# Optimization experiments

Measured on AMD Instinct MI355X. Metric: run time of the kernel, lower is better.

The kernel has to match this reference:

```python
import jax, jax.numpy as jnp
import numpy as np

B, T, E = 4, 2048, 1024
H = 16
DH = E // H
SCALE = DH ** -0.5


def setup_inputs() -> dict:
    key = jax.random.key(0)
    ks = jax.random.split(key, 5)
    # small init scale for weights to keep softmax well-conditioned
    return {
        "x": jax.random.normal(ks[0], (B, T, E), dtype=jnp.float32),
        "w_qkv": jax.random.normal(ks[1], (3 * E, E), dtype=jnp.float32) * 0.02,
        "b_qkv": jax.random.normal(ks[2], (3 * E,), dtype=jnp.float32) * 0.02,
        "w_proj": jax.random.normal(ks[3], (E, E), dtype=jnp.float32) * 0.02,
        "b_proj": jax.random.normal(ks[4], (E,), dtype=jnp.float32) * 0.02,
    }


def reference(x, w_qkv, b_qkv, w_proj, b_proj):
    Bs, Ts, Es = x.shape
    # fused qkv projection (torch Linear: y = x W^T + b)
    qkv = x @ w_qkv.T + b_qkv                       # [B,T,3E]
    qkv = qkv.reshape(Bs, Ts, 3, H, DH)
    q, k, v = qkv[:, :, 0], qkv[:, :, 1], qkv[:, :, 2]  # [B,T,H,DH]
    # scores: materialize full TxT matrix per head, as in the original
    scores = jnp.einsum("bthd,bshd->bhts", q, k) * SCALE  # [B,H,T,T]
    causal = jnp.tril(jnp.ones((Ts, Ts), dtype=bool))
    scores = jnp.where(causal[None, None], scores, jnp.float32(-jnp.inf))
    attn = jax.nn.softmax(scores, axis=-1)
    # dropout = 0.0 (eval / deterministic reference)
    out = jnp.einsum("bhts,bshd->bthd", attn, v)    # [B,T,H,DH]
    out = out.reshape(Bs, Ts, Es)
    return out @ w_proj.T + b_proj
```

## Files before the change

### kernel.cpp

```cpp
#include <hip/hip_runtime.h>
#include <hip/hip_bf16.h>

#define B_ 4
#define T_ 2048
#define E_ 1024
#define H_ 16
#define DH_ 64
#define QSCALE_ 0.18033688f

typedef __attribute__((ext_vector_type(8))) short bf16x8;
typedef __attribute__((ext_vector_type(4))) float f32x4;
typedef unsigned int u32;

__device__ inline ushort f2bf(float f) {
    union { float f; unsigned u; } v; v.f = f;
    unsigned r = (v.u + 0x7fffu + ((v.u >> 16) & 1u)) >> 16;
    return (ushort)r;
}

__device__ inline u32 pack2bf(float a, float b) {
    union { float f; u32 u; } ua, ub; ua.f = a; ub.f = b;
    return __builtin_amdgcn_perm(ub.u, ua.u, 0x07060302);
}

__device__ inline void gload16(const ushort* g, ushort* l) {
    __builtin_amdgcn_global_load_lds((const __attribute__((address_space(1))) u32*)g,
                                     (__attribute__((address_space(3))) u32*)l, 16, 0, 0);
}

__global__ void cvt_all(const float* __restrict__ x, const float* __restrict__ wq,
                        const float* __restrict__ wp,
                        ushort* __restrict__ xo, ushort* __restrict__ wqo, ushort* __restrict__ wpo)
{
    const int NX = B_ * T_ * E_ / 4;
    const int NW = 3 * E_ * E_ / 4;
    int i = blockIdx.x * 256 + threadIdx.x;
    const float* s; ushort* d; int off;
    if (i < NX)            { s = x;  d = xo;  off = i; }
    else if (i < NX + NW)  { s = wq; d = wqo; off = i - NX; }
    else                   { s = wp; d = wpo; off = i - NX - NW; }
    float4 f = ((const float4*)s)[off];
    ushort4 u;
    u.x = f2bf(f.x); u.y = f2bf(f.y); u.z = f2bf(f.z); u.w = f2bf(f.w);
    ((ushort4*)d)[off] = u;
}

__global__ __launch_bounds__(256) void gemm_qkv(
    const ushort* __restrict__ Xb, const ushort* __restrict__ Wb,
    const float* __restrict__ bias,
    ushort* __restrict__ Q, ushort* __restrict__ K, ushort* __restrict__ Vt)
{
    __shared__ ushort As[128 * 64];
    __shared__ ushort Bs[128 * 64];
    const int m0 = blockIdx.x * 128;
    const int n0 = blockIdx.y * 128;
    const int kind = n0 >> 10;
    const int tid  = threadIdx.x;
    const int wave = tid >> 6, lane = tid & 63;
    const int lrow = lane & 15, quad = lane >> 4;
    const int srow8 = lane >> 3;
    const int scol8 = ((lane & 7) ^ srow8) * 8;

    const ushort* gA = Xb + (size_t)(m0 + wave * 8 + srow8) * 1024 + scol8;
    const ushort* gB = Wb + (size_t)(n0 + wave * 8 + srow8) * 1024 + scol8;

    const int mw = (wave >> 1) * 64, nw = (wave & 1) * 64;
    const int rsw = (lrow & 7);

    f32x4 acc[4][4];
#pragma unroll
    for (int i = 0; i < 4; i++)
#pragma unroll
        for (int j = 0; j < 4; j++) acc[i][j] = f32x4{0.f, 0.f, 0.f, 0.f};

    const int b = m0 >> 11;
    const bool ct = (kind != 2);

    for (int k0 = 0; k0 < 1024; k0 += 64) {
        __syncthreads();
#pragma unroll
        for (int g = 0; g < 4; g++) {
            gload16(gA + (size_t)g * 32 * 1024 + k0, &As[(g * 32 + wave * 8) * 64]);
            gload16(gB + (size_t)g * 32 * 1024 + k0, &Bs[(g * 32 + wave * 8) * 64]);
        }
        __syncthreads();
#pragma unroll
        for (int ks = 0; ks < 2; ks++) {
            const int usw = ((ks * 4 + quad) ^ rsw) * 8;
            bf16x8 a[4], bfr[4];
#pragma unroll
            for (int i = 0; i < 4; i++)
                a[i] = *(const bf16x8*)&As[(mw + i * 16 + lrow) * 64 + usw];
#pragma unroll
            for (int j = 0; j < 4; j++)
                bfr[j] = *(const bf16x8*)&Bs[(nw + j * 16 + lrow) * 64 + usw];
            if (ct) {
#pragma unroll
                for (int i = 0; i < 4; i++)
#pragma unroll
                    for (int j = 0; j < 4; j++)
                        acc[i][j] = __builtin_amdgcn_mfma_f32_16x16x32_bf16(bfr[j], a[i], acc[i][j], 0, 0, 0);
            } else {
#pragma unroll
                for (int i = 0; i < 4; i++)
#pragma unroll
                    for (int j = 0; j < 4; j++)
                        acc[i][j] = __builtin_amdgcn_mfma_f32_16x16x32_bf16(a[i], bfr[j], acc[i][j], 0, 0, 0);
            }
        }
    }

    if (ct) {
        ushort* dst = (kind == 0) ? Q : K;
        const float scale = (kind == 0) ? QSCALE_ : 1.f;
#pragma unroll
        for (int j = 0; j < 4; j++) {
            int nq = (n0 & 1023) + nw + j * 16 + quad * 4;
            int h = nq >> 6, d = nq & 63;
            float4 bv = *(const float4*)&bias[n0 + nw + j * 16 + quad * 4];
            size_t bh = (size_t)(b * H_ + h);
#pragma unroll
            for (int i = 0; i < 4; i++) {
                int t = (m0 + mw + i * 16 + lrow) & 2047;
                ushort4 o;
                o.x = f2bf((acc[i][j][0] + bv.x) * scale);
                o.y = f2bf((acc[i][j][1] + bv.y) * scale);
                o.z = f2bf((acc[i][j][2] + bv.z) * scale);
                o.w = f2bf((acc[i][j][3] + bv.w) * scale);
                *(ushort4*)&dst[(bh * T_ + t) * DH_ + d] = o;
            }
        }
    } else {
#pragma unroll
        for (int j = 0; j < 4; j++) {
            int nv = (n0 & 1023) + nw + j * 16 + lrow;
            int h = nv >> 6, d = nv & 63;
            float bv = bias[n0 + nw + j * 16 + lrow];
            size_t bh = (size_t)(b * H_ + h);
#pragma unroll
            for (int i = 0; i < 4; i++) {
                int t = (m0 + mw + i * 16 + quad * 4) & 2047;
                ushort4 o;
                o.x = f2bf(acc[i][j][0] + bv);
                o.y = f2bf(acc[i][j][1] + bv);
                o.z = f2bf(acc[i][j][2] + bv);
                o.w = f2bf(acc[i][j][3] + bv);
                *(ushort4*)&Vt[(bh * DH_ + d) * T_ + t] = o;
            }
        }
    }
}

#define LDT_ 76

__global__ __launch_bounds__(256) void flash_attn(
    const ushort* __restrict__ Q, const ushort* __restrict__ K,
    const ushort* __restrict__ Vg,
    ushort* __restrict__ O)
{
    __shared__ ushort Ks[64 * LDT_];
    __shared__ ushort Vt[64 * LDT_];
    __shared__ ushort Ps[128 * LDT_];

    const int qtA = 15 - blockIdx.x;
    const int qtB = blockIdx.x;
    const int bh = blockIdx.y;
    const int tid  = threadIdx.x;
    const int wave = tid >> 6, lane = tid & 63;
    const int lrow = lane & 15, quad = lane >> 4;
    const int sr = tid >> 2, sc = (tid & 3) * 16;

    const ushort* Qbh = Q  + (size_t)bh * T_ * DH_;
    const ushort* Kbh = K  + (size_t)bh * T_ * DH_;
    const ushort* Vbh = Vg + (size_t)bh * DH_ * T_;
    const int b_ = bh >> 4, h_ = bh & 15;

    auto stageQ = [&](int qt, bf16x8 qa[2][2]) {
        int qr = tid >> 1, qc = (tid & 1) * 32;
        const ushort* src = &Qbh[(size_t)(qt * 128 + qr) * DH_ + qc];
#pragma unroll
        for (int i = 0; i < 4; i++)
            *(int4*)&Ps[qr * LDT_ + qc + 8 * i] = *(const int4*)&src[8 * i];
        __syncthreads();
#pragma unroll
        for (int s = 0; s < 2; s++)
#pragma unroll
            for (int h = 0; h < 2; h++)
                qa[s][h] = *(const bf16x8*)&Ps[(s * 64 + wave * 16 + lrow) * LDT_ + h * 32 + quad * 8];
    };

    bf16x8 qaA[2][2], qaB[2][2];
    stageQ(qtA, qaA);
    __syncthreads();
    stageQ(qtB, qaB);

    auto run = [&](const bf16x8 (&qa)[2][2], int qt) {
        const int lastkt = 2 * qt + 1;

        int4 kr0 = *(const int4*)&Kbh[(size_t)sr * DH_ + sc];
        int4 kr1 = *(const int4*)&Kbh[(size_t)sr * DH_ + sc + 8];
        int4 vr0 = *(const int4*)&Vbh[(size_t)sr * T_ + sc];
        int4 vr1 = *(const int4*)&Vbh[(size_t)sr * T_ + sc + 8];

        float ls[2] = {0.f, 0.f};
        f32x4 accO[2][4];
#pragma unroll
        for (int s = 0; s < 2; s++)
#pragma unroll
            for (int j = 0; j < 4; j++) accO[s][j] = f32x4{0.f, 0.f, 0.f, 0.f};

        for (int kt = 0; kt <= lastkt; ++kt) {
            __syncthreads();
            *(int4*)&Ks[sr * LDT_ + sc]     = kr0;
            *(int4*)&Ks[sr * LDT_ + sc + 8] = kr1;
            *(int4*)&Vt[sr * LDT_ + sc]     = vr0;
            *(int4*)&Vt[sr * LDT_ + sc + 8] = vr1;
            __syncthreads();
            if (kt < lastkt) {
                kr0 = *(const int4*)&Kbh[(size_t)((kt + 1) * 64 + sr) * DH_ + sc];
                kr1 = *(const int4*)&Kbh[(size_t)((kt + 1) * 64 + sr) * DH_ + sc + 8];
                vr0 = *(const int4*)&Vbh[(size_t)sr * T_ + (kt + 1) * 64 + sc];
                vr1 = *(const int4*)&Vbh[(size_t)sr * T_ + (kt + 1) * 64 + sc + 8];
            }

            bf16x8 kb0[4], kb1[4];
#pragma unroll
            for (int j = 0; j < 4; j++) {
                kb0[j] = *(const bf16x8*)&Ks[(j * 16 + lrow) * LDT_ + quad * 8];
                kb1[j] = *(const bf16x8*)&Ks[(j * 16 + lrow) * LDT_ + 32 + quad * 8];
            }

            const bool do0 = (kt != lastkt);
#pragma unroll
            for (int s = 0; s < 2; s++) {
                if (s == 0 && !do0) continue;
                f32x4 st[4];
#pragma unroll
                for (int j = 0; j < 4; j++) {
                    f32x4 sj = f32x4{0.f, 0.f, 0.f, 0.f};
                    sj = __builtin_amdgcn_mfma_f32_16x16x32_bf16(kb0[j], qa[s][0], sj, 0, 0, 0);
                    sj = __builtin_amdgcn_mfma_f32_16x16x32_bf16(kb1[j], qa[s][1], sj, 0, 0, 0);
                    st[j] = sj;
                }
                if (kt == 2 * qt + s) {
                    const int qrow = qt * 128 + s * 64 + wave * 16 + lrow;
                    const int keyb = kt * 64 + quad * 4;
#pragma unroll
                    for (int j = 0; j < 4; j++)
#pragma unroll
                        for (int r = 0; r < 4; r++)
                            if (keyb + j * 16 + r > qrow) st[j][r] = -1e30f;
                }
                float lp = 0.f;
#pragma unroll
                for (int j = 0; j < 4; j++)
#pragma unroll
                    for (int r = 0; r < 4; r++) {
                        float p = __builtin_amdgcn_exp2f(st[j][r]);
                        st[j][r] = p;
                        lp += p;
                    }
                ls[s] += lp;
                ushort* prow = &Ps[(s * 64 + wave * 16 + lrow) * LDT_ + quad * 4];
#pragma unroll
                for (int j = 0; j < 4; j++) {
                    *(u32*)&prow[j * 16]     = pack2bf(st[j][0], st[j][1]);
                    *(u32*)&prow[j * 16 + 2] = pack2bf(st[j][2], st[j][3]);
                }
            }

            bf16x8 vb0[4], vb1[4];
#pragma unroll
            for (int j = 0; j < 4; j++) {
                vb0[j] = *(const bf16x8*)&Vt[(j * 16 + lrow) * LDT_ + quad * 8];
                vb1[j] = *(const bf16x8*)&Vt[(j * 16 + lrow) * LDT_ + 32 + quad * 8];
            }
#pragma unroll
            for (int s = 0; s < 2; s++) {
                if (s == 0 && !do0) continue;
                bf16x8 pa0 = *(const bf16x8*)&Ps[(s * 64 + wave * 16 + lrow) * LDT_ + quad * 8];
                bf16x8 pa1 = *(const bf16x8*)&Ps[(s * 64 + wave * 16 + lrow) * LDT_ + 32 + quad * 8];
#pragma unroll
                for (int jd = 0; jd < 4; jd++) {
                    accO[s][jd] = __builtin_amdgcn_mfma_f32_16x16x32_bf16(pa0, vb0[jd], accO[s][jd], 0, 0, 0);
                    accO[s][jd] = __builtin_amdgcn_mfma_f32_16x16x32_bf16(pa1, vb1[jd], accO[s][jd], 0, 0, 0);
                }
            }
        }

#pragma unroll
        for (int s = 0; s < 2; s++) {
            ls[s] += __shfl_xor(ls[s], 16, 64);
            ls[s] += __shfl_xor(ls[s], 32, 64);
        }
#pragma unroll
        for (int s = 0; s < 2; s++) {
#pragma unroll
            for (int r = 0; r < 4; r++) {
                float lv = __shfl(ls[s], quad * 4 + r, 64);
                float inv = 1.f / lv;
                int t = qt * 128 + s * 64 + wave * 16 + quad * 4 + r;
#pragma unroll
                for (int jd = 0; jd < 4; jd++) {
                    int d = jd * 16 + lrow;
                    O[((size_t)(b_ * T_ + t)) * E_ + h_ * DH_ + d] = f2bf(accO[s][jd][r] * inv);
                }
            }
        }
    };

    run(qaA, qtA);
    run(qaB, qtB);
}

__global__ __launch_bounds__(256) void gemm_proj(
    const ushort* __restrict__ Ob, const ushort* __restrict__ Wb,
    const float* __restrict__ bias, float* __restrict__ out)
{
    __shared__ ushort As[128 * 64];
    __shared__ ushort Bs[128 * 64];
    const int m0 = blockIdx.x * 128;
    const int n0 = blockIdx.y * 128;
    const int tid  = threadIdx.x;
    const int wave = tid >> 6, lane = tid & 63;
    const int lrow = lane & 15, quad = lane >> 4;
    const int srow8 = lane >> 3;
    const int scol8 = ((lane & 7) ^ srow8) * 8;

    const ushort* gA = Ob + (size_t)(m0 + wave * 8 + srow8) * 1024 + scol8;
    const ushort* gB = Wb + (size_t)(n0 + wave * 8 + srow8) * 1024 + scol8;

    const int mw = (wave >> 1) * 64, nw = (wave & 1) * 64;
    const int rsw = (lrow & 7);

    f32x4 acc[4][4];
#pragma unroll
    for (int i = 0; i < 4; i++)
#pragma unroll
        for (int j = 0; j < 4; j++) acc[i][j] = f32x4{0.f, 0.f, 0.f, 0.f};

    for (int k0 = 0; k0 < 1024; k0 += 64) {
        __syncthreads();
#pragma unroll
        for (int g = 0; g < 4; g++) {
            gload16(gA + (size_t)g * 32 * 1024 + k0, &As[(g * 32 + wave * 8) * 64]);
            gload16(gB + (size_t)g * 32 * 1024 + k0, &Bs[(g * 32 + wave * 8) * 64]);
        }
        __syncthreads();
#pragma unroll
        for (int ks = 0; ks < 2; ks++) {
            const int usw = ((ks * 4 + quad) ^ rsw) * 8;
            bf16x8 a[4], bfr[4];
#pragma unroll
            for (int i = 0; i < 4; i++)
                a[i] = *(const bf16x8*)&As[(mw + i * 16 + lrow) * 64 + usw];
#pragma unroll
            for (int j = 0; j < 4; j++)
                bfr[j] = *(const bf16x8*)&Bs[(nw + j * 16 + lrow) * 64 + usw];
#pragma unroll
            for (int i = 0; i < 4; i++)
#pragma unroll
                for (int j = 0; j < 4; j++)
                    acc[i][j] = __builtin_amdgcn_mfma_f32_16x16x32_bf16(bfr[j], a[i], acc[i][j], 0, 0, 0);
        }
    }

#pragma unroll
    for (int j = 0; j < 4; j++) {
        int n = n0 + nw + j * 16 + quad * 4;
        float4 bv = *(const float4*)&bias[n];
#pragma unroll
        for (int i = 0; i < 4; i++) {
            int m = m0 + mw + i * 16 + lrow;
            float4 o;
            o.x = acc[i][j][0] + bv.x;
            o.y = acc[i][j][1] + bv.y;
            o.z = acc[i][j][2] + bv.z;
            o.w = acc[i][j][3] + bv.w;
            *(float4*)&out[(size_t)m * 1024 + n] = o;
        }
    }
}

extern "C" void kernel_launch(void* const* d_in, const int* in_sizes, int n_in,
                              void* d_out, int out_size, void* d_ws, size_t ws_size,
                              hipStream_t stream) {
    const float* x      = (const float*)d_in[0];
    const float* w_qkv  = (const float*)d_in[1];
    const float* b_qkv  = (const float*)d_in[2];
    const float* w_proj = (const float*)d_in[3];
    const float* b_proj = (const float*)d_in[4];
    float* out = (float*)d_out;

    char* ws = (char*)d_ws;
    ushort* Xb     = (ushort*)ws; ws += (size_t)B_ * T_ * E_ * 2;
    ushort* Wqkvb  = (ushort*)ws; ws += (size_t)3 * E_ * E_ * 2;
    ushort* Wprojb = (ushort*)ws; ws += (size_t)E_ * E_ * 2;
    ushort* Qb     = (ushort*)ws; ws += (size_t)B_ * H_ * T_ * DH_ * 2;
    ushort* Kb     = (ushort*)ws; ws += (size_t)B_ * H_ * T_ * DH_ * 2;
    ushort* Vtb    = (ushort*)ws; ws += (size_t)B_ * H_ * T_ * DH_ * 2;
    ushort* Ob     = (ushort*)ws; ws += (size_t)B_ * T_ * E_ * 2;

    int ntot = (B_ * T_ * E_ + 3 * E_ * E_ + E_ * E_) / 4;
    cvt_all<<<ntot / 256, 256, 0, stream>>>(x, w_qkv, w_proj, Xb, Wqkvb, Wprojb);

    gemm_qkv<<<dim3(64, 24), 256, 0, stream>>>(Xb, Wqkvb, b_qkv, Qb, Kb, Vtb);
    flash_attn<<<dim3(8, 64), 256, 0, stream>>>(Qb, Kb, Vtb, Ob);
    gemm_proj<<<dim3(64, 8), 256, 0, stream>>>(Ob, Wprojb, b_proj, out);
}
```

Baseline: 241.5 us.

## Pipeline QKV and projection GEMMs with 4-stage LDS ring and 512-thread blocks

Rewrites both bf16 GEMM kernels to use 256x128 tiles with 8 waves and a 4-slot shared-memory ring of K=32 slices. Global loads for slice t+3 are issued while slice t is consumed, with explicit vmcnt waits, raw s_barrier and sched_barrier fences, and raised wave priority around the MFMA block. This is meant to hide global-load latency that the previous load-sync-compute loop exposed. The cost is more LDS per block and fragile hand-placed wait counts that must match the number of loads in flight.

```diff
diff --git a/kernel.cpp b/kernel.cpp
--- a/kernel.cpp
+++ b/kernel.cpp
@@ -45,83 +45,103 @@
     ((ushort4*)d)[off] = u;
 }
 
-__global__ __launch_bounds__(256) void gemm_qkv(
+
+#define STAGE3(t_) { const int ss_ = (t_) & 3; const int sk_ = (t_) * 32;      \
+    gload16(gA0 + sk_, &As[ss_][wave * 512]);                                  \
+    gload16(gA1 + sk_, &As[ss_][4096 + wave * 512]);                           \
+    gload16(gB0 + sk_, &Bs[ss_][wave * 512]); }
+
+#define GPHASE(t_, vmstr_, DOSTAGE_, ...) do {                                 \
+    const int seg_ = (t_) & 3;                                                 \
+    bf16x8 afr[4], bfr[4];                                                     \
+    _Pragma("unroll") for (int i_ = 0; i_ < 4; i_++)                           \
+        afr[i_] = *(const bf16x8*)&As[seg_][(mbase + i_ * 16 + lrow) * 32 + usw]; \
+    _Pragma("unroll") for (int j_ = 0; j_ < 4; j_++)                           \
+        bfr[j_] = *(const bf16x8*)&Bs[seg_][(nbase + j_ * 16 + lrow) * 32 + usw]; \
+    if (DOSTAGE_) STAGE3((t_) + 3);                                            \
+    asm volatile("s_waitcnt " vmstr_ ::: "memory");                            \
+    __builtin_amdgcn_s_barrier();                                              \
+    asm volatile("s_waitcnt lgkmcnt(0)" ::: "memory");                         \
+    __builtin_amdgcn_sched_barrier(0);                                         \
+    __builtin_amdgcn_s_setprio(1);                                             \
+    __VA_ARGS__                                                                \
+    __builtin_amdgcn_s_setprio(0);                                             \
+    __builtin_amdgcn_sched_barrier(0);                                         \
+    __builtin_amdgcn_s_barrier();                                              \
+    __builtin_amdgcn_sched_barrier(0);                                         \
+} while (0)
+
+#define MFMA_QKV                                                               \
+    if (ct) {                                                                  \
+        _Pragma("unroll") for (int i_ = 0; i_ < 4; i_++)                       \
+        _Pragma("unroll") for (int j_ = 0; j_ < 4; j_++)                       \
+            acc[i_][j_] = __builtin_amdgcn_mfma_f32_16x16x32_bf16(bfr[j_], afr[i_], acc[i_][j_], 0, 0, 0); \
+    } else {                                                                   \
+        _Pragma("unroll") for (int i_ = 0; i_ < 4; i_++)                       \
+        _Pragma("unroll") for (int j_ = 0; j_ < 4; j_++)                       \
+            acc[i_][j_] = __builtin_amdgcn_mfma_f32_16x16x32_bf16(afr[i_], bfr[j_], acc[i_][j_], 0, 0, 0); \
+    }
+
+#define MFMA_CT                                                                \
+    _Pragma("unroll") for (int i_ = 0; i_ < 4; i_++)                           \
+    _Pragma("unroll") for (int j_ = 0; j_ < 4; j_++)                           \
+        acc[i_][j_] = __builtin_amdgcn_mfma_f32_16x16x32_bf16(bfr[j_], afr[i_], acc[i_][j_], 0, 0, 0);
+
+__global__ __launch_bounds__(512, 2) void gemm_qkv(
     const ushort* __restrict__ Xb, const ushort* __restrict__ Wb,
     const float* __restrict__ bias,
     ushort* __restrict__ Q, ushort* __restrict__ K, ushort* __restrict__ Vt)
 {
-    __shared__ ushort As[128 * 64];
-    __shared__ ushort Bs[128 * 64];
-    const int m0 = blockIdx.x * 128;
+    __shared__ ushort As[4][256 * 32];
+    __shared__ ushort Bs[4][128 * 32];
+    const int m0 = blockIdx.x * 256;
     const int n0 = blockIdx.y * 128;
     const int kind = n0 >> 10;
     const int tid  = threadIdx.x;
     const int wave = tid >> 6, lane = tid & 63;
     const int lrow = lane & 15, quad = lane >> 4;
-    const int srow8 = lane >> 3;
-    const int scol8 = ((lane & 7) ^ srow8) * 8;
-
-    const ushort* gA = Xb + (size_t)(m0 + wave * 8 + srow8) * 1024 + scol8;
-    const ushort* gB = Wb + (size_t)(n0 + wave * 8 + srow8) * 1024 + scol8;
-
-    const int mw = (wave >> 1) * 64, nw = (wave & 1) * 64;
-    const int rsw = (lrow & 7);
-
-    f32x4 acc[4][4];
-#pragma unroll
-    for (int i = 0; i < 4; i++)
-#pragma unroll
-        for (int j = 0; j < 4; j++) acc[i][j] = f32x4{0.f, 0.f, 0.f, 0.f};
+    const int mbase = (wave >> 1) * 64;
+    const int nbase = (wave & 1) * 64;
+    const int usw = (quad ^ (lrow & 3)) * 8;
+    const int sR = lane >> 2;
+    const int su = ((lane & 3) ^ (sR & 3)) * 8;
+
+    const ushort* gA0 = Xb + (size_t)(m0 + wave * 16 + sR) * 1024 + su;
+    const ushort* gA1 = gA0 + (size_t)128 * 1024;
+    const ushort* gB0 = Wb + (size_t)(n0 + wave * 16 + sR) * 1024 + su;
 
     const int b = m0 >> 11;
     const bool ct = (kind != 2);
 
-    for (int k0 = 0; k0 < 1024; k0 += 64) {
-        __syncthreads();
-#pragma unroll
-        for (int g = 0; g < 4; g++) {
-            gload16(gA + (size_t)g * 32 * 1024 + k0, &As[(g * 32 + wave * 8) * 64]);
-            gload16(gB + (size_t)g * 32 * 1024 + k0, &Bs[(g * 32 + wave * 8) * 64]);
-        }
-        __syncthreads();
-#pragma unroll
-        for (int ks = 0; ks < 2; ks++) {
-            const int usw = ((ks * 4 + quad) ^ rsw) * 8;
-            bf16x8 a[4], bfr[4];
-#pragma unroll
-            for (int i = 0; i < 4; i++)
-                a[i] = *(const bf16x8*)&As[(mw + i * 16 + lrow) * 64 + usw];
-#pragma unroll
-            for (int j = 0; j < 4; j++)
-                bfr[j] = *(const bf16x8*)&Bs[(nw + j * 16 + lrow) * 64 + usw];
-            if (ct) {
-#pragma unroll
-                for (int i = 0; i < 4; i++)
-#pragma unroll
-                    for (int j = 0; j < 4; j++)
-                        acc[i][j] = __builtin_amdgcn_mfma_f32_16x16x32_bf16(bfr[j], a[i], acc[i][j], 0, 0, 0);
-            } else {
-#pragma unroll
-                for (int i = 0; i < 4; i++)
-#pragma unroll
-                    for (int j = 0; j < 4; j++)
-                        acc[i][j] = __builtin_amdgcn_mfma_f32_16x16x32_bf16(a[i], bfr[j], acc[i][j], 0, 0, 0);
-            }
-        }
-    }
+    f32x4 acc[4][4];
+#pragma unroll
+    for (int i = 0; i < 4; i++)
+#pragma unroll
+        for (int j = 0; j < 4; j++) acc[i][j] = f32x4{0.f, 0.f, 0.f, 0.f};
+
+    STAGE3(0); STAGE3(1); STAGE3(2);
+    asm volatile("s_waitcnt vmcnt(6)" ::: "memory");
+    __builtin_amdgcn_s_barrier();
+    __builtin_amdgcn_sched_barrier(0);
+
+#pragma unroll 4
+    for (int t = 0; t < 29; t++) GPHASE(t, "vmcnt(6)", 1, MFMA_QKV);
+    GPHASE(29, "vmcnt(3)", 0, MFMA_QKV);
+    GPHASE(30, "vmcnt(0)", 0, MFMA_QKV);
+    GPHASE(31, "vmcnt(0)", 0, MFMA_QKV);
 
     if (ct) {
         ushort* dst = (kind == 0) ? Q : K;
         const float scale = (kind == 0) ? QSCALE_ : 1.f;
 #pragma unroll
         for (int j = 0; j < 4; j++) {
-            int nq = (n0 & 1023) + nw + j * 16 + quad * 4;
+            int nq = (n0 & 1023) + nbase + j * 16 + quad * 4;
             int h = nq >> 6, d = nq & 63;
-            float4 bv = *(const float4*)&bias[n0 + nw + j * 16 + quad * 4];
+            float4 bv = *(const float4*)&bias[n0 + nbase + j * 16 + quad * 4];
             size_t bh = (size_t)(b * H_ + h);
 #pragma unroll
             for (int i = 0; i < 4; i++) {
-                int t = (m0 + mw + i * 16 + lrow) & 2047;
+                int t = (m0 + mbase + i * 16 + lrow) & 2047;
                 ushort4 o;
                 o.x = f2bf((acc[i][j][0] + bv.x) * scale);
                 o.y = f2bf((acc[i][j][1] + bv.y) * scale);
@@ -133,13 +153,13 @@
     } else {
 #pragma unroll
         for (int j = 0; j < 4; j++) {
-            int nv = (n0 & 1023) + nw + j * 16 + lrow;
+            int nv = (n0 & 1023) + nbase + j * 16 + lrow;
             int h = nv >> 6, d = nv & 63;
-            float bv = bias[n0 + nw + j * 16 + lrow];
+            float bv = bias[n0 + nbase + j * 16 + lrow];
             size_t bh = (size_t)(b * H_ + h);
 #pragma unroll
             for (int i = 0; i < 4; i++) {
-                int t = (m0 + mw + i * 16 + quad * 4) & 2047;
+                int t = (m0 + mbase + i * 16 + quad * 4) & 2047;
                 ushort4 o;
                 o.x = f2bf(acc[i][j][0] + bv);
                 o.y = f2bf(acc[i][j][1] + bv);
@@ -313,25 +333,26 @@
     run(qaB, qtB);
 }
 
-__global__ __launch_bounds__(256) void gemm_proj(
+__global__ __launch_bounds__(512, 2) void gemm_proj(
     const ushort* __restrict__ Ob, const ushort* __restrict__ Wb,
     const float* __restrict__ bias, float* __restrict__ out)
 {
-    __shared__ ushort As[128 * 64];
-    __shared__ ushort Bs[128 * 64];
-    const int m0 = blockIdx.x * 128;
+    __shared__ ushort As[4][256 * 32];
+    __shared__ ushort Bs[4][128 * 32];
+    const int m0 = blockIdx.x * 256;
     const int n0 = blockIdx.y * 128;
     const int tid  = threadIdx.x;
     const int wave = tid >> 6, lane = tid & 63;
     const int lrow = lane & 15, quad = lane >> 4;
-    const int srow8 = lane >> 3;
-    const int scol8 = ((lane & 7) ^ srow8) * 8;
-
-    const ushort* gA = Ob + (size_t)(m0 + wave * 8 + srow8) * 1024 + scol8;
-    const ushort* gB = Wb + (size_t)(n0 + wave * 8 + srow8) * 1024 + scol8;
-
-    const int mw = (wave >> 1) * 64, nw = (wave & 1) * 64;
-    const int rsw = (lrow & 7);
+    const int mbase = (wave >> 1) * 64;
+    const int nbase = (wave & 1) * 64;
+    const int usw = (quad ^ (lrow & 3)) * 8;
+    const int sR = lane >> 2;
+    const int su = ((lane & 3) ^ (sR & 3)) * 8;
+
+    const ushort* gA0 = Ob + (size_t)(m0 + wave * 16 + sR) * 1024 + su;
+    const ushort* gA1 = gA0 + (size_t)128 * 1024;
+    const ushort* gB0 = Wb + (size_t)(n0 + wave * 16 + sR) * 1024 + su;
 
     f32x4 acc[4][4];
 #pragma unroll
@@ -339,39 +360,24 @@
 #pragma unroll
         for (int j = 0; j < 4; j++) acc[i][j] = f32x4{0.f, 0.f, 0.f, 0.f};
 
-    for (int k0 = 0; k0 < 1024; k0 += 64) {
-        __syncthreads();
-#pragma unroll
-        for (int g = 0; g < 4; g++) {
-            gload16(gA + (size_t)g * 32 * 1024 + k0, &As[(g * 32 + wave * 8) * 64]);
-            gload16(gB + (size_t)g * 32 * 1024 + k0, &Bs[(g * 32 + wave * 8) * 64]);
-        }
-        __syncthreads();
-#pragma unroll
-        for (int ks = 0; ks < 2; ks++) {
-            const int usw = ((ks * 4 + quad) ^ rsw) * 8;
-            bf16x8 a[4], bfr[4];
-#pragma unroll
-            for (int i = 0; i < 4; i++)
-                a[i] = *(const bf16x8*)&As[(mw + i * 16 + lrow) * 64 + usw];
-#pragma unroll
-            for (int j = 0; j < 4; j++)
-                bfr[j] = *(const bf16x8*)&Bs[(nw + j * 16 + lrow) * 64 + usw];
-#pragma unroll
-            for (int i = 0; i < 4; i++)
-#pragma unroll
-                for (int j = 0; j < 4; j++)
-                    acc[i][j] = __builtin_amdgcn_mfma_f32_16x16x32_bf16(bfr[j], a[i], acc[i][j], 0, 0, 0);
-        }
-    }
+    STAGE3(0); STAGE3(1); STAGE3(2);
+    asm volatile("s_waitcnt vmcnt(6)" ::: "memory");
+    __builtin_amdgcn_s_barrier();
+    __builtin_amdgcn_sched_barrier(0);
+
+#pragma unroll 4
+    for (int t = 0; t < 29; t++) GPHASE(t, "vmcnt(6)", 1, MFMA_CT);
+    GPHASE(29, "vmcnt(3)", 0, MFMA_CT);
+    GPHASE(30, "vmcnt(0)", 0, MFMA_CT);
+    GPHASE(31, "vmcnt(0)", 0, MFMA_CT);
 
 #pragma unroll
     for (int j = 0; j < 4; j++) {
-        int n = n0 + nw + j * 16 + quad * 4;
+        int n = n0 + nbase + j * 16 + quad * 4;
         float4 bv = *(const float4*)&bias[n];
 #pragma unroll
         for (int i = 0; i < 4; i++) {
-            int m = m0 + mw + i * 16 + lrow;
+            int m = m0 + mbase + i * 16 + lrow;
             float4 o;
             o.x = acc[i][j][0] + bv.x;
             o.y = acc[i][j][1] + bv.y;
@@ -404,7 +410,7 @@
     int ntot = (B_ * T_ * E_ + 3 * E_ * E_ + E_ * E_) / 4;
     cvt_all<<<ntot / 256, 256, 0, stream>>>(x, w_qkv, w_proj, Xb, Wqkvb, Wprojb);
 
-    gemm_qkv<<<dim3(64, 24), 256, 0, stream>>>(Xb, Wqkvb, b_qkv, Qb, Kb, Vtb);
+    gemm_qkv<<<dim3(32, 24), 512, 0, stream>>>(Xb, Wqkvb, b_qkv, Qb, Kb, Vtb);
     flash_attn<<<dim3(8, 64), 256, 0, stream>>>(Qb, Kb, Vtb, Ob);
-    gemm_proj<<<dim3(64, 8), 256, 0, stream>>>(Ob, Wprojb, b_proj, out);
-}
+    gemm_proj<<<dim3(32, 8), 512, 0, stream>>>(Ob, Wprojb, b_proj, out);
+}
```

After: 259.2 us. 7.3% more time.

## Share one K/V sweep between both query tiles in attention kernel

Applied to the files above, without the earlier changes.

Both query tiles now run inside a single loop over key/value tiles instead of two separate sequential passes. Each K/V tile is loaded from global memory and staged to LDS once, then used for both tiles; the second tile takes part only while its causal limit has not been reached. This roughly halves K/V global traffic and barrier count for the block. The cost is two output accumulator sets and two Q fragment sets live at once, which raises register pressure and may lower occupancy.

```diff
diff --git a/kernel.cpp b/kernel.cpp
--- a/kernel.cpp
+++ b/kernel.cpp
@@ -194,100 +194,120 @@
     __syncthreads();
     stageQ(qtB, qaB);
 
-    auto run = [&](const bf16x8 (&qa)[2][2], int qt) {
-        const int lastkt = 2 * qt + 1;
-
-        int4 kr0 = *(const int4*)&Kbh[(size_t)sr * DH_ + sc];
-        int4 kr1 = *(const int4*)&Kbh[(size_t)sr * DH_ + sc + 8];
-        int4 vr0 = *(const int4*)&Vbh[(size_t)sr * T_ + sc];
-        int4 vr1 = *(const int4*)&Vbh[(size_t)sr * T_ + sc + 8];
-
-        float ls[2] = {0.f, 0.f};
-        f32x4 accO[2][4];
-#pragma unroll
-        for (int s = 0; s < 2; s++)
-#pragma unroll
-            for (int j = 0; j < 4; j++) accO[s][j] = f32x4{0.f, 0.f, 0.f, 0.f};
-
-        for (int kt = 0; kt <= lastkt; ++kt) {
-            __syncthreads();
-            *(int4*)&Ks[sr * LDT_ + sc]     = kr0;
-            *(int4*)&Ks[sr * LDT_ + sc + 8] = kr1;
-            *(int4*)&Vt[sr * LDT_ + sc]     = vr0;
-            *(int4*)&Vt[sr * LDT_ + sc + 8] = vr1;
-            __syncthreads();
-            if (kt < lastkt) {
-                kr0 = *(const int4*)&Kbh[(size_t)((kt + 1) * 64 + sr) * DH_ + sc];
-                kr1 = *(const int4*)&Kbh[(size_t)((kt + 1) * 64 + sr) * DH_ + sc + 8];
-                vr0 = *(const int4*)&Vbh[(size_t)sr * T_ + (kt + 1) * 64 + sc];
-                vr1 = *(const int4*)&Vbh[(size_t)sr * T_ + (kt + 1) * 64 + sc + 8];
-            }
-
-            bf16x8 kb0[4], kb1[4];
+    const int lastA = 2 * qtA + 1;
+    const int lastB = 2 * qtB + 1;
+
+    int4 kr0 = *(const int4*)&Kbh[(size_t)sr * DH_ + sc];
+    int4 kr1 = *(const int4*)&Kbh[(size_t)sr * DH_ + sc + 8];
+    int4 vr0 = *(const int4*)&Vbh[(size_t)sr * T_ + sc];
+    int4 vr1 = *(const int4*)&Vbh[(size_t)sr * T_ + sc + 8];
+
+    float lsA[2] = {0.f, 0.f}, lsB[2] = {0.f, 0.f};
+    f32x4 accA[2][4], accB[2][4];
+#pragma unroll
+    for (int s = 0; s < 2; s++)
+#pragma unroll
+        for (int j = 0; j < 4; j++) {
+            accA[s][j] = f32x4{0.f, 0.f, 0.f, 0.f};
+            accB[s][j] = f32x4{0.f, 0.f, 0.f, 0.f};
+        }
+
+    auto qk_step = [&](const bf16x8 (&qa)[2][2], const bf16x8 (&kb0)[4], const bf16x8 (&kb1)[4],
+                       float (&ls)[2], int qt, int kt, bool do0) {
+#pragma unroll
+        for (int s = 0; s < 2; s++) {
+            if (s == 0 && !do0) continue;
+            f32x4 st[4];
 #pragma unroll
             for (int j = 0; j < 4; j++) {
-                kb0[j] = *(const bf16x8*)&Ks[(j * 16 + lrow) * LDT_ + quad * 8];
-                kb1[j] = *(const bf16x8*)&Ks[(j * 16 + lrow) * LDT_ + 32 + quad * 8];
-            }
-
-            const bool do0 = (kt != lastkt);
-#pragma unroll
-            for (int s = 0; s < 2; s++) {
-                if (s == 0 && !do0) continue;
-                f32x4 st[4];
-#pragma unroll
-                for (int j = 0; j < 4; j++) {
-                    f32x4 sj = f32x4{0.f, 0.f, 0.f, 0.f};
-                    sj = __builtin_amdgcn_mfma_f32_16x16x32_bf16(kb0[j], qa[s][0], sj, 0, 0, 0);
-                    sj = __builtin_amdgcn_mfma_f32_16x16x32_bf16(kb1[j], qa[s][1], sj, 0, 0, 0);
-                    st[j] = sj;
+                f32x4 sj = f32x4{0.f, 0.f, 0.f, 0.f};
+                sj = __builtin_amdgcn_mfma_f32_16x16x32_bf16(kb0[j], qa[s][0], sj, 0, 0, 0);
+                sj = __builtin_amdgcn_mfma_f32_16x16x32_bf16(kb1[j], qa[s][1], sj, 0, 0, 0);
+                st[j] = sj;
+            }
+            if (kt == 2 * qt + s) {
+                const int qrow = qt * 128 + s * 64 + wave * 16 + lrow;
+                const int keyb = kt * 64 + quad * 4;
+#pragma unroll
+                for (int j = 0; j < 4; j++)
+#pragma unroll
+                    for (int r = 0; r < 4; r++)
+                        if (keyb + j * 16 + r > qrow) st[j][r] = -1e30f;
+            }
+            float lp = 0.f;
+#pragma unroll
+            for (int j = 0; j < 4; j++)
+#pragma unroll
+                for (int r = 0; r < 4; r++) {
+                    float p = __builtin_amdgcn_exp2f(st[j][r]);
+                    st[j][r] = p;
+                    lp += p;
                 }
-                if (kt == 2 * qt + s) {
-                    const int qrow = qt * 128 + s * 64 + wave * 16 + lrow;
-                    const int keyb = kt * 64 + quad * 4;
-#pragma unroll
-                    for (int j = 0; j < 4; j++)
-#pragma unroll
-                        for (int r = 0; r < 4; r++)
-                            if (keyb + j * 16 + r > qrow) st[j][r] = -1e30f;
-                }
-                float lp = 0.f;
-#pragma unroll
-                for (int j = 0; j < 4; j++)
-#pragma unroll
-                    for (int r = 0; r < 4; r++) {
-                        float p = __builtin_amdgcn_exp2f(st[j][r]);
-                        st[j][r] = p;
-                        lp += p;
-                    }
-                ls[s] += lp;
-                ushort* prow = &Ps[(s * 64 + wave * 16 + lrow) * LDT_ + quad * 4];
-#pragma unroll
-                for (int j = 0; j < 4; j++) {
-                    *(u32*)&prow[j * 16]     = pack2bf(st[j][0], st[j][1]);
-                    *(u32*)&prow[j * 16 + 2] = pack2bf(st[j][2], st[j][3]);
-                }
-            }
-
-            bf16x8 vb0[4], vb1[4];
+            ls[s] += lp;
+            ushort* prow = &Ps[(s * 64 + wave * 16 + lrow) * LDT_ + quad * 4];
 #pragma unroll
             for (int j = 0; j < 4; j++) {
-                vb0[j] = *(const bf16x8*)&Vt[(j * 16 + lrow) * LDT_ + quad * 8];
-                vb1[j] = *(const bf16x8*)&Vt[(j * 16 + lrow) * LDT_ + 32 + quad * 8];
-            }
-#pragma unroll
-            for (int s = 0; s < 2; s++) {
-                if (s == 0 && !do0) continue;
-                bf16x8 pa0 = *(const bf16x8*)&Ps[(s * 64 + wave * 16 + lrow) * LDT_ + quad * 8];
-                bf16x8 pa1 = *(const bf16x8*)&Ps[(s * 64 + wave * 16 + lrow) * LDT_ + 32 + quad * 8];
-#pragma unroll
-                for (int jd = 0; jd < 4; jd++) {
-                    accO[s][jd] = __builtin_amdgcn_mfma_f32_16x16x32_bf16(pa0, vb0[jd], accO[s][jd], 0, 0, 0);
-                    accO[s][jd] = __builtin_amdgcn_mfma_f32_16x16x32_bf16(pa1, vb1[jd], accO[s][jd], 0, 0, 0);
-                }
-            }
-        }
-
+                *(u32*)&prow[j * 16]     = pack2bf(st[j][0], st[j][1]);
+                *(u32*)&prow[j * 16 + 2] = pack2bf(st[j][2], st[j][3]);
+            }
+        }
+    };
+
+    auto pv_step = [&](const bf16x8 (&vb0)[4], const bf16x8 (&vb1)[4],
+                       f32x4 (&acc)[2][4], bool do0) {
+#pragma unroll
+        for (int s = 0; s < 2; s++) {
+            if (s == 0 && !do0) continue;
+            bf16x8 pa0 = *(const bf16x8*)&Ps[(s * 64 + wave * 16 + lrow) * LDT_ + quad * 8];
+            bf16x8 pa1 = *(const bf16x8*)&Ps[(s * 64 + wave * 16 + lrow) * LDT_ + 32 + quad * 8];
+#pragma unroll
+            for (int jd = 0; jd < 4; jd++) {
+                acc[s][jd] = __builtin_amdgcn_mfma_f32_16x16x32_bf16(pa0, vb0[jd], acc[s][jd], 0, 0, 0);
+                acc[s][jd] = __builtin_amdgcn_mfma_f32_16x16x32_bf16(pa1, vb1[jd], acc[s][jd], 0, 0, 0);
+            }
+        }
+    };
+
+    for (int kt = 0; kt <= lastA; ++kt) {
+        __syncthreads();
+        *(int4*)&Ks[sr * LDT_ + sc]     = kr0;
+        *(int4*)&Ks[sr * LDT_ + sc + 8] = kr1;
+        *(int4*)&Vt[sr * LDT_ + sc]     = vr0;
+        *(int4*)&Vt[sr * LDT_ + sc + 8] = vr1;
+        __syncthreads();
+        if (kt < lastA) {
+            kr0 = *(const int4*)&Kbh[(size_t)((kt + 1) * 64 + sr) * DH_ + sc];
+            kr1 = *(const int4*)&Kbh[(size_t)((kt + 1) * 64 + sr) * DH_ + sc + 8];
+            vr0 = *(const int4*)&Vbh[(size_t)sr * T_ + (kt + 1) * 64 + sc];
+            vr1 = *(const int4*)&Vbh[(size_t)sr * T_ + (kt + 1) * 64 + sc + 8];
+        }
+
+        bf16x8 kb0[4], kb1[4];
+#pragma unroll
+        for (int j = 0; j < 4; j++) {
+            kb0[j] = *(const bf16x8*)&Ks[(j * 16 + lrow) * LDT_ + quad * 8];
+            kb1[j] = *(const bf16x8*)&Ks[(j * 16 + lrow) * LDT_ + 32 + quad * 8];
+        }
+
+        const bool doA0 = (kt != lastA);
+        qk_step(qaA, kb0, kb1, lsA, qtA, kt, doA0);
+
+        bf16x8 vb0[4], vb1[4];
+#pragma unroll
+        for (int j = 0; j < 4; j++) {
+            vb0[j] = *(const bf16x8*)&Vt[(j * 16 + lrow) * LDT_ + quad * 8];
+            vb1[j] = *(const bf16x8*)&Vt[(j * 16 + lrow) * LDT_ + 32 + quad * 8];
+        }
+        pv_step(vb0, vb1, accA, doA0);
+
+        if (kt <= lastB) {
+            const bool doB0 = (kt != lastB);
+            qk_step(qaB, kb0, kb1, lsB, qtB, kt, doB0);
+            pv_step(vb0, vb1, accB, doB0);
+        }
+    }
+
+    auto epilogue = [&](float (&ls)[2], f32x4 (&acc)[2][4], int qt) {
 #pragma unroll
         for (int s = 0; s < 2; s++) {
             ls[s] += __shfl_xor(ls[s], 16, 64);
@@ -303,14 +323,14 @@
 #pragma unroll
                 for (int jd = 0; jd < 4; jd++) {
                     int d = jd * 16 + lrow;
-                    O[((size_t)(b_ * T_ + t)) * E_ + h_ * DH_ + d] = f2bf(accO[s][jd][r] * inv);
+                    O[((size_t)(b_ * T_ + t)) * E_ + h_ * DH_ + d] = f2bf(acc[s][jd][r] * inv);
                 }
             }
         }
     };
 
-    run(qaA, qtA);
-    run(qaB, qtB);
+    epilogue(lsA, accA, qtA);
+    epilogue(lsB, accB, qtB);
 }
 
 __global__ __launch_bounds__(256) void gemm_proj(
```

After: 265.8 us. 10.1% more time.

## Load K/V MFMA fragments directly from global memory instead of LDS staging

Applied to the files above, without the earlier changes.

Removes the shared-memory K and V tiles, the register prefetch of the next tile, and the two block-wide barriers per key tile. Each wave now reads its K and V MFMA operands straight from global memory, relying on the L1/L2 caches to serve the repeated reads across the four waves. Q staging for the second query tile moves to after the first tile's run, behind a barrier. This cuts LDS traffic and synchronisation and frees LDS for occupancy. In exchange it gives up the software prefetch, so global load latency is exposed at the start of each iteration, and each K/V tile is fetched four times per block.

```diff
diff --git a/kernel.cpp b/kernel.cpp
--- a/kernel.cpp
+++ b/kernel.cpp
@@ -158,8 +158,6 @@
     const ushort* __restrict__ Vg,
     ushort* __restrict__ O)
 {
-    __shared__ ushort Ks[64 * LDT_];
-    __shared__ ushort Vt[64 * LDT_];
     __shared__ ushort Ps[128 * LDT_];
 
     const int qtA = 15 - blockIdx.x;
@@ -168,7 +166,6 @@
     const int tid  = threadIdx.x;
     const int wave = tid >> 6, lane = tid & 63;
     const int lrow = lane & 15, quad = lane >> 4;
-    const int sr = tid >> 2, sc = (tid & 3) * 16;
 
     const ushort* Qbh = Q  + (size_t)bh * T_ * DH_;
     const ushort* Kbh = K  + (size_t)bh * T_ * DH_;
@@ -189,19 +186,9 @@
                 qa[s][h] = *(const bf16x8*)&Ps[(s * 64 + wave * 16 + lrow) * LDT_ + h * 32 + quad * 8];
     };
 
-    bf16x8 qaA[2][2], qaB[2][2];
-    stageQ(qtA, qaA);
-    __syncthreads();
-    stageQ(qtB, qaB);
-
     auto run = [&](const bf16x8 (&qa)[2][2], int qt) {
         const int lastkt = 2 * qt + 1;
 
-        int4 kr0 = *(const int4*)&Kbh[(size_t)sr * DH_ + sc];
-        int4 kr1 = *(const int4*)&Kbh[(size_t)sr * DH_ + sc + 8];
-        int4 vr0 = *(const int4*)&Vbh[(size_t)sr * T_ + sc];
-        int4 vr1 = *(const int4*)&Vbh[(size_t)sr * T_ + sc + 8];
-
         float ls[2] = {0.f, 0.f};
         f32x4 accO[2][4];
 #pragma unroll
@@ -209,25 +196,19 @@
 #pragma unroll
             for (int j = 0; j < 4; j++) accO[s][j] = f32x4{0.f, 0.f, 0.f, 0.f};
 
+        const ushort* Kl = Kbh + (size_t)lrow * DH_ + quad * 8;
+        const ushort* Vl = Vbh + (size_t)lrow * T_ + quad * 8;
+
         for (int kt = 0; kt <= lastkt; ++kt) {
-            __syncthreads();
-            *(int4*)&Ks[sr * LDT_ + sc]     = kr0;
-            *(int4*)&Ks[sr * LDT_ + sc + 8] = kr1;
-            *(int4*)&Vt[sr * LDT_ + sc]     = vr0;
-            *(int4*)&Vt[sr * LDT_ + sc + 8] = vr1;
-            __syncthreads();
-            if (kt < lastkt) {
-                kr0 = *(const int4*)&Kbh[(size_t)((kt + 1) * 64 + sr) * DH_ + sc];
-                kr1 = *(const int4*)&Kbh[(size_t)((kt + 1) * 64 + sr) * DH_ + sc + 8];
-                vr0 = *(const int4*)&Vbh[(size_t)sr * T_ + (kt + 1) * 64 + sc];
-                vr1 = *(const int4*)&Vbh[(size_t)sr * T_ + (kt + 1) * 64 + sc + 8];
-            }
-
-            bf16x8 kb0[4], kb1[4];
+            bf16x8 kb0[4], kb1[4], vb0[4], vb1[4];
 #pragma unroll
             for (int j = 0; j < 4; j++) {
-                kb0[j] = *(const bf16x8*)&Ks[(j * 16 + lrow) * LDT_ + quad * 8];
-                kb1[j] = *(const bf16x8*)&Ks[(j * 16 + lrow) * LDT_ + 32 + quad * 8];
+                const ushort* kp = Kl + (size_t)(kt * 64 + j * 16) * DH_;
+                kb0[j] = *(const bf16x8*)kp;
+                kb1[j] = *(const bf16x8*)(kp + 32);
+                const ushort* vp = Vl + (size_t)(j * 16) * T_ + kt * 64;
+                vb0[j] = *(const bf16x8*)vp;
+                vb1[j] = *(const bf16x8*)(vp + 32);
             }
 
             const bool do0 = (kt != lastkt);
@@ -269,12 +250,6 @@
                 }
             }
 
-            bf16x8 vb0[4], vb1[4];
-#pragma unroll
-            for (int j = 0; j < 4; j++) {
-                vb0[j] = *(const bf16x8*)&Vt[(j * 16 + lrow) * LDT_ + quad * 8];
-                vb1[j] = *(const bf16x8*)&Vt[(j * 16 + lrow) * LDT_ + 32 + quad * 8];
-            }
 #pragma unroll
             for (int s = 0; s < 2; s++) {
                 if (s == 0 && !do0) continue;
@@ -309,7 +284,12 @@
         }
     };
 
+    bf16x8 qaA[2][2];
+    stageQ(qtA, qaA);
     run(qaA, qtA);
+    __syncthreads();
+    bf16x8 qaB[2][2];
+    stageQ(qtB, qaB);
     run(qaB, qtB);
 }
 
```

After: 310.0 us. 1.28x slower.
